# Kernel tuning notes

Measured on AMD Instinct MI355X. Metric: run time of the kernel, lower is better.

## Reference

```python
import jax, jax.numpy as jnp
import numpy as np

N, E, D, C = 100000, 3200000, 256, 47


def _l2norm(x):
    n = jnp.sqrt(jnp.sum(x * x, axis=-1, keepdims=True))
    return x / jnp.maximum(n, 1e-12)


def setup_inputs() -> dict:
    key = jax.random.key(0)
    ks = jax.random.split(key, 12)
    w = lambda k, s: jax.random.normal(k, s, dtype=jnp.float32) * 0.05
    return {
        "x": jax.random.normal(ks[0], (N, D), dtype=jnp.float32),
        "src": jax.random.randint(ks[1], (E,), 0, N, dtype=jnp.int32),
        "dst": jnp.sort(jax.random.randint(ks[2], (E,), 0, N, dtype=jnp.int32)),
        "W_pre": w(ks[3], (D, D)), "b_pre": jnp.zeros((D,), jnp.float32),
        "Wl1": w(ks[4], (D, D)), "bl1": jnp.zeros((D,), jnp.float32),
        "Wr1": w(ks[5], (D, D)),
        "Wl2": w(ks[6], (D, D)), "bl2": jnp.zeros((D,), jnp.float32),
        "Wr2": w(ks[7], (D, D)),
        "W_jk": w(ks[8], (D, D)), "b_jk": jnp.zeros((D,), jnp.float32),
        "W_post": w(ks[9], (C, D)), "b_post": jnp.zeros((C,), jnp.float32),
    }


def _sage_conv(x, src, dst, Wl, bl, Wr):
    # aggr='add': m_i = sum_{j in N(i)} x_j  (SpMM as gather + segment_sum)
    m = jax.ops.segment_sum(x[src], dst, num_segments=N)
    out = m @ Wl.T + bl + x @ Wr.T  # lin_l(aggr) + lin_r(root)
    return _l2norm(out)            # SAGEConv normalize=True


def reference(x, src, dst, W_pre, b_pre, Wl1, bl1, Wr1, Wl2, bl2, Wr2,
              W_jk, b_jk, W_post, b_post):
    # pre-MLP (1 layer) + classifier activation; dropout=0, batch_norm off
    h = jax.nn.relu(x @ W_pre.T + b_pre)
    h = _l2norm(h)  # self.normalize
    # GraphSAGE, jk='last': act+dropout after every conv, then jk lin
    h = jax.nn.relu(_sage_conv(h, src, dst, Wl1, bl1, Wr1))
    h = jax.nn.relu(_sage_conv(h, src, dst, Wl2, bl2, Wr2))
    h = h @ W_jk.T + b_jk
    # post: act + post-MLP (1 layer)
    h = jax.nn.relu(h)
    h = h @ W_post.T + b_post
    return jax.nn.log_softmax(h, axis=-1)
```

## Files before the change

### kernel.cpp

```cpp
#include <hip/hip_runtime.h>
#include <stdint.h>

#define DEV __device__ __forceinline__

typedef __attribute__((ext_vector_type(8))) short bh8;
typedef __attribute__((ext_vector_type(4))) float f4;
#define LDS_AS __attribute__((address_space(3)))
#define GLB_AS __attribute__((address_space(1)))

DEV unsigned short f2bf(float f) {
    union { float f; uint32_t u; } c; c.f = f;
    uint32_t u = c.u;
    uint32_t r = (u + 0x7fffu + ((u >> 16) & 1u)) >> 16;
    return (unsigned short)r;
}
DEV float bf2f(unsigned short h) {
    union { uint32_t u; float f; } c; c.u = ((uint32_t)h) << 16;
    return c.f;
}

DEV uint8_t f2fp8(float v) {
    const float vs = v * 256.f;
    union { float f; uint32_t u; } c; c.f = vs;
    const uint32_t u = c.u + 0x7ffffu + ((c.u >> 20) & 1u);
    const uint32_t f8 = (u >> 20) - 960u;
    return (vs < 0.015625f) ? (uint8_t)0 : (uint8_t)f8;
}
DEV float fp8w(uint32_t x) { union { uint32_t u; float f; } c; c.u = x; return c.f; }

DEV void gload16(const void* g, void* l) {
    __builtin_amdgcn_global_load_lds((const GLB_AS uint32_t*)g, (LDS_AS uint32_t*)l, 16, 0, 0);
}

__global__ __launch_bounds__(256) void prep_kernel(
    const float* __restrict__ w0, const float* __restrict__ w1, const float* __restrict__ w2,
    const float* __restrict__ w3, const float* __restrict__ w4, const float* __restrict__ w5,
    unsigned short* __restrict__ wbBase,
    const int* __restrict__ dst, int* __restrict__ rp, int N, int E) {
    const int b = blockIdx.x;
    if (b < 384) {
        const int wi = b >> 6;
        const int i = (b & 63) * 256 + threadIdx.x;
        const float* s = wi == 0 ? w0 : wi == 1 ? w1 : wi == 2 ? w2 : wi == 3 ? w3 : wi == 4 ? w4 : w5;
        const float4 v = ((const float4*)s)[i];
        ushort4 o; o.x = f2bf(v.x); o.y = f2bf(v.y); o.z = f2bf(v.z); o.w = f2bf(v.w);
        ((ushort4*)(wbBase + (size_t)wi * 65536))[i] = o;
    } else {
        const int i = (b - 384) * 256 + threadIdx.x;
        if (i <= N) {
            int lo = 0, hi = E;
            while (lo < hi) { int mid = (lo + hi) >> 1; if (dst[mid] < i) lo = mid + 1; else hi = mid; }
            rp[i] = lo;
        }
    }
}

__global__ __launch_bounds__(256) void agg_fp8_kernel(const uint32_t* __restrict__ h32,
                                                      const int* __restrict__ src,
                                                      const int* __restrict__ rp,
                                                      unsigned short* __restrict__ mout, int nNodes) {
    const int node = blockIdx.x * 4 + (threadIdx.x >> 6);
    if (node >= nNodes) return;
    const int lane = threadIdx.x & 63;
    const int beg = __builtin_amdgcn_readfirstlane(rp[node]);
    const int end = __builtin_amdgcn_readfirstlane(rp[node + 1]);
    float a0 = 0.f, a1 = 0.f, a2 = 0.f, a3 = 0.f;
    int e = beg;
    for (; e + 8 <= end; e += 8) {
        int s[8];
#pragma unroll
        for (int i = 0; i < 8; i++) s[i] = src[e + i];
        uint32_t w[8];
#pragma unroll
        for (int i = 0; i < 8; i++) w[i] = h32[(size_t)s[i] * 64 + lane];
#pragma unroll
        for (int i = 0; i < 8; i++) {
            a0 += fp8w((w[i] << 20) & 0x07f00000u);
            a1 += fp8w((w[i] << 12) & 0x07f00000u);
            a2 += fp8w((w[i] << 4)  & 0x07f00000u);
            a3 += fp8w((w[i] >> 4)  & 0x07f00000u);
        }
    }
    for (; e < end; ++e) {
        const uint32_t w = h32[(size_t)src[e] * 64 + lane];
        a0 += fp8w((w << 20) & 0x07f00000u);
        a1 += fp8w((w << 12) & 0x07f00000u);
        a2 += fp8w((w << 4)  & 0x07f00000u);
        a3 += fp8w((w >> 4)  & 0x07f00000u);
    }
    const float sc = 0x1p112f;
    ushort4 o;
    o.x = f2bf(a0 * sc); o.y = f2bf(a1 * sc); o.z = f2bf(a2 * sc); o.w = f2bf(a3 * sc);
    *(ushort4*)&mout[(size_t)node * 256 + (size_t)lane * 4] = o;
}

__global__ __launch_bounds__(256) void agg_kernel(const unsigned short* __restrict__ h,
                                                  const int* __restrict__ src,
                                                  const int* __restrict__ rp,
                                                  unsigned short* __restrict__ mout, int nNodes) {
    const int node = blockIdx.x * 4 + (threadIdx.x >> 6);
    if (node >= nNodes) return;
    const int lane = threadIdx.x & 63;
    const size_t fo = (size_t)lane * 4;
    const int beg = __builtin_amdgcn_readfirstlane(rp[node]);
    const int end = __builtin_amdgcn_readfirstlane(rp[node + 1]);
    float a0 = 0.f, a1 = 0.f, a2 = 0.f, a3 = 0.f;
    int e = beg;
    for (; e + 4 <= end; e += 4) {
        const int s0 = src[e], s1 = src[e+1], s2 = src[e+2], s3 = src[e+3];
        ushort4 v0 = *(const ushort4*)&h[(size_t)s0 * 256 + fo];
        ushort4 v1 = *(const ushort4*)&h[(size_t)s1 * 256 + fo];
        ushort4 v2 = *(const ushort4*)&h[(size_t)s2 * 256 + fo];
        ushort4 v3 = *(const ushort4*)&h[(size_t)s3 * 256 + fo];
        a0 += bf2f(v0.x) + bf2f(v1.x) + bf2f(v2.x) + bf2f(v3.x);
        a1 += bf2f(v0.y) + bf2f(v1.y) + bf2f(v2.y) + bf2f(v3.y);
        a2 += bf2f(v0.z) + bf2f(v1.z) + bf2f(v2.z) + bf2f(v3.z);
        a3 += bf2f(v0.w) + bf2f(v1.w) + bf2f(v2.w) + bf2f(v3.w);
    }
    for (; e < end; ++e) {
        const int s = src[e];
        ushort4 v = *(const ushort4*)&h[(size_t)s * 256 + fo];
        a0 += bf2f(v.x); a1 += bf2f(v.y); a2 += bf2f(v.z); a3 += bf2f(v.w);
    }
    ushort4 o;
    o.x = f2bf(a0); o.y = f2bf(a1); o.z = f2bf(a2); o.w = f2bf(a3);
    *(ushort4*)&mout[(size_t)node * 256 + fo] = o;
}

template <int NSEG, int EPMODE, bool EMIT, bool CVT>
__global__ __launch_bounds__(512) void gemm_kernel(
    const void* __restrict__ A0v, const unsigned short* __restrict__ A1,
    const unsigned short* __restrict__ B0, const unsigned short* __restrict__ B1,
    const float* __restrict__ bias, unsigned short* __restrict__ Out,
    uint8_t* __restrict__ F8, int M) {
    __shared__ unsigned short Alds[2 * 128 * 32];
    __shared__ unsigned short Blds[2 * 256 * 32];
    __shared__ float ssq_lds[8][64];

    const unsigned short* A0 = (const unsigned short*)A0v;
    const float* A0f = (const float*)A0v;

    const int t = threadIdx.x;
    const int wid = t >> 6;
    const int lane = t & 63;
    const int wr = wid >> 2, wc = wid & 3;
    const int l15 = lane & 15;
    const int kh = lane >> 4;
    const int rowBase = blockIdx.x * 128;

    f4 acc[4][4];
#pragma unroll
    for (int m = 0; m < 4; m++)
#pragma unroll
        for (int n = 0; n < 4; n++) acc[m][n] = f4{0.f, 0.f, 0.f, 0.f};

    const int rA = t >> 2;
    const int sSlotA = (t & 3) ^ ((rA >> 1) & 3);
    int grA = rowBase + rA; if (grA > M - 1) grA = M - 1;
    const size_t gAoff = (size_t)grA * 256 + sSlotA * 8;
    const size_t gBoff0 = (size_t)rA * 256 + sSlotA * 8;
    const size_t gBoff1 = (size_t)(128 + rA) * 256 + sSlotA * 8;

    const int nsteps = NSEG * 8;
    auto STAGE = [&](int s, int buf) {
        const unsigned short* Bp = (NSEG == 2 && s >= 8) ? B1 : B0;
        const int k0 = (s & 7) * 32;
        if (CVT) {
            const float* Af = A0f + gAoff + k0;
            const float4 v0 = *(const float4*)Af;
            const float4 v1 = *(const float4*)(Af + 4);
            bh8 o;
            o[0] = (short)f2bf(v0.x); o[1] = (short)f2bf(v0.y);
            o[2] = (short)f2bf(v0.z); o[3] = (short)f2bf(v0.w);
            o[4] = (short)f2bf(v1.x); o[5] = (short)f2bf(v1.y);
            o[6] = (short)f2bf(v1.z); o[7] = (short)f2bf(v1.w);
            *(bh8*)&Alds[buf * 4096 + wid * 512 + lane * 8] = o;
        } else {
            const unsigned short* Ap = (NSEG == 2 && s >= 8) ? A1 : A0;
            gload16(Ap + gAoff + k0, &Alds[buf * 4096 + wid * 512]);
        }
        gload16(Bp + gBoff0 + k0, &Blds[buf * 8192 + wid * 512]);
        gload16(Bp + gBoff1 + k0, &Blds[buf * 8192 + 4096 + wid * 512]);
    };

    STAGE(0, 0);
    asm volatile("s_waitcnt vmcnt(0)" ::: "memory");
    __syncthreads();

#pragma unroll 2
    for (int s = 0; s < nsteps; ++s) {
        const int cur = s & 1;
        if (s + 1 < nsteps) STAGE(s + 1, cur ^ 1);
        bh8 a[4], b[4];
#pragma unroll
        for (int m = 0; m < 4; m++) {
            const int ra = wr * 64 + m * 16 + l15;
            a[m] = *(const bh8*)&Alds[cur * 4096 + ra * 32 + ((kh ^ ((ra >> 1) & 3)) * 8)];
        }
#pragma unroll
        for (int n = 0; n < 4; n++) {
            const int rb = wc * 64 + n * 16 + l15;
            b[n] = *(const bh8*)&Blds[cur * 8192 + rb * 32 + ((kh ^ ((rb >> 1) & 3)) * 8)];
        }
#pragma unroll
        for (int m = 0; m < 4; m++)
#pragma unroll
            for (int n = 0; n < 4; n++)
                acc[m][n] = __builtin_amdgcn_mfma_f32_16x16x32_bf16(a[m], b[n], acc[m][n], 0, 0, 0);
        asm volatile("s_waitcnt vmcnt(0)" ::: "memory");
        __syncthreads();
    }

    const int cBase = wc * 64 + l15;
    float sq[4][4];
#pragma unroll
    for (int m = 0; m < 4; m++) { sq[m][0] = 0.f; sq[m][1] = 0.f; sq[m][2] = 0.f; sq[m][3] = 0.f; }
#pragma unroll
    for (int n = 0; n < 4; n++) {
        const float bv = bias[cBase + n * 16];
#pragma unroll
        for (int m = 0; m < 4; m++)
#pragma unroll
            for (int r = 0; r < 4; r++) {
                float v = acc[m][n][r] + bv;
                if (EPMODE != 1) v = fmaxf(v, 0.f);
                acc[m][n][r] = v;
                sq[m][r] += v * v;
            }
    }

    if (EPMODE != 2) {
#pragma unroll
        for (int mask = 1; mask < 16; mask <<= 1)
#pragma unroll
            for (int m = 0; m < 4; m++)
#pragma unroll
                for (int r = 0; r < 4; r++) sq[m][r] += __shfl_xor(sq[m][r], mask);
        if (l15 == 0) {
#pragma unroll
            for (int m = 0; m < 4; m++)
#pragma unroll
                for (int r = 0; r < 4; r++) ssq_lds[wid][m * 16 + kh * 4 + r] = sq[m][r];
        }
        __syncthreads();
#pragma unroll
        for (int m = 0; m < 4; m++)
#pragma unroll
            for (int r = 0; r < 4; r++) {
                const int rr = m * 16 + kh * 4 + r;
                const float s = ssq_lds[wr * 4 + 0][rr] + ssq_lds[wr * 4 + 1][rr] +
                                ssq_lds[wr * 4 + 2][rr] + ssq_lds[wr * 4 + 3][rr];
                sq[m][r] = 1.f / fmaxf(sqrtf(s), 1e-12f);
            }
    }

#pragma unroll
    for (int m = 0; m < 4; m++)
#pragma unroll
        for (int r = 0; r < 4; r++) {
            const int grow = rowBase + wr * 64 + m * 16 + kh * 4 + r;
            if (grow < M) {
#pragma unroll
                for (int n = 0; n < 4; n++) {
                    float v = acc[m][n][r];
                    if (EPMODE != 2) v *= sq[m][r];
                    if (EPMODE == 1) v = fmaxf(v, 0.f);
                    Out[(size_t)grow * 256 + cBase + n * 16] = f2bf(v);
                    if (EMIT) F8[(size_t)grow * 256 + cBase + n * 16] = f2fp8(v);
                }
            }
        }
}

__global__ __launch_bounds__(256) void jkfinal_kernel(
    const unsigned short* __restrict__ A,
    const unsigned short* __restrict__ Bjk,
    const float* __restrict__ bjk,
    const float* __restrict__ Wp, const float* __restrict__ bp,
    float* __restrict__ out, int M) {
    __shared__ unsigned short S[20480];
    __shared__ unsigned short Tlds[64 * 256];

    const int t = threadIdx.x;
    const int wid = t >> 6;
    const int lane = t & 63;
    const int wc = wid;
    const int l15 = lane & 15;
    const int kh = lane >> 4;
    const int rowBase = blockIdx.x * 64;

    f4 acc[4][4];
#pragma unroll
    for (int m = 0; m < 4; m++)
#pragma unroll
        for (int n = 0; n < 4; n++) acc[m][n] = f4{0.f, 0.f, 0.f, 0.f};

    const int rA = t >> 2;
    const int sSlotA = (t & 3) ^ ((rA >> 1) & 3);
    int grA = rowBase + rA; if (grA > M - 1) grA = M - 1;
    const size_t gAoff = (size_t)grA * 256 + sSlotA * 8;
    const size_t gBoff = (size_t)rA * 256 + sSlotA * 8;

    auto STAGE = [&](int s, int buf) {
        const int k0 = s * 32;
        gload16(A + gAoff + k0, &S[buf * 2048 + wid * 512]);
#pragma unroll
        for (int p = 0; p < 4; ++p)
            gload16(Bjk + (size_t)p * 16384 + gBoff + k0,
                    &S[4096 + buf * 8192 + p * 2048 + wid * 512]);
    };

    STAGE(0, 0);
    asm volatile("s_waitcnt vmcnt(0)" ::: "memory");
    __syncthreads();

#pragma unroll 2
    for (int s = 0; s < 8; ++s) {
        const int cur = s & 1;
        if (s + 1 < 8) STAGE(s + 1, cur ^ 1);
        bh8 a[4], b[4];
#pragma unroll
        for (int m = 0; m < 4; m++) {
            const int ra = m * 16 + l15;
            a[m] = *(const bh8*)&S[cur * 2048 + ra * 32 + ((kh ^ ((ra >> 1) & 3)) * 8)];
        }
#pragma unroll
        for (int n = 0; n < 4; n++) {
            const int rb = wc * 64 + n * 16 + l15;
            b[n] = *(const bh8*)&S[4096 + cur * 8192 + rb * 32 + ((kh ^ ((rb >> 1) & 3)) * 8)];
        }
#pragma unroll
        for (int m = 0; m < 4; m++)
#pragma unroll
            for (int n = 0; n < 4; n++)
                acc[m][n] = __builtin_amdgcn_mfma_f32_16x16x32_bf16(a[m], b[n], acc[m][n], 0, 0, 0);
        asm volatile("s_waitcnt vmcnt(0)" ::: "memory");
        __syncthreads();
    }

    const int cBase = wc * 64 + l15;
#pragma unroll
    for (int n = 0; n < 4; n++) {
        const float bv = bjk[cBase + n * 16];
        const int slot = wc * 4 + n;
#pragma unroll
        for (int m = 0; m < 4; m++)
#pragma unroll
            for (int r = 0; r < 4; r++) {
                const int row = m * 16 + kh * 4 + r;
                const float v = fmaxf(acc[m][n][r] + bv, 0.f);
                Tlds[row * 256 + (((slot ^ ((row >> 2) & 7)) << 4) | l15)] = f2bf(v);
            }
    }
    for (int i = t; i < 48 * 32; i += 256) {
        const int rb = i >> 5, slot = i & 31;
        bh8 o;
        if (rb < 47) {
#pragma unroll
            for (int j = 0; j < 8; j++) o[j] = (short)f2bf(Wp[rb * 256 + slot * 8 + j]);
        } else {
#pragma unroll
            for (int j = 0; j < 8; j++) o[j] = 0;
        }
        *(bh8*)&S[rb * 256 + ((slot ^ (rb & 7)) * 8)] = o;
    }
    __syncthreads();

    const int lrow = wid * 16 + l15;
    bh8 a2[8];
#pragma unroll
    for (int ks = 0; ks < 8; ks++) {
        const int slot = ks * 2 + (kh >> 1);
        a2[ks] = *(const bh8*)&Tlds[lrow * 256 + (((slot ^ ((lrow >> 2) & 7)) << 4) | ((kh & 1) * 8))];
    }
    f4 acc2[3];
#pragma unroll
    for (int n = 0; n < 3; n++) acc2[n] = f4{0.f, 0.f, 0.f, 0.f};
#pragma unroll
    for (int ks = 0; ks < 8; ks++)
#pragma unroll
        for (int n = 0; n < 3; n++) {
            const int rb = n * 16 + l15;
            const bh8 b = *(const bh8*)&S[rb * 256 + (((ks * 4 + kh) ^ (rb & 7)) * 8)];
            acc2[n] = __builtin_amdgcn_mfma_f32_16x16x32_bf16(a2[ks], b, acc2[n], 0, 0, 0);
        }

    const int c0 = l15, c1 = 16 + l15, c2 = 32 + l15;
    const float b0 = bp[c0], b1 = bp[c1];
    const float b2 = (l15 < 15) ? bp[c2] : 0.f;
#pragma unroll
    for (int r = 0; r < 4; r++) {
        const int grow = rowBase + wid * 16 + kh * 4 + r;
        const float x0 = acc2[0][r] + b0;
        const float x1 = acc2[1][r] + b1;
        const float x2 = (l15 < 15) ? (acc2[2][r] + b2) : -3.0e38f;
        float mx = fmaxf(fmaxf(x0, x1), x2);
#pragma unroll
        for (int msk = 1; msk < 16; msk <<= 1) mx = fmaxf(mx, __shfl_xor(mx, msk));
        float se = __expf(x0 - mx) + __expf(x1 - mx) + ((l15 < 15) ? __expf(x2 - mx) : 0.f);
#pragma unroll
        for (int msk = 1; msk < 16; msk <<= 1) se += __shfl_xor(se, msk);
        const float ls = __logf(se) + mx;
        if (grow < M) {
            float* orow = &out[(size_t)grow * 47];
            orow[c0] = x0 - ls;
            orow[c1] = x1 - ls;
            if (l15 < 15) orow[c2] = x2 - ls;
        }
    }
}

extern "C" void kernel_launch(void* const* d_in, const int* in_sizes, int n_in,
                              void* d_out, int out_size, void* d_ws, size_t ws_size,
                              hipStream_t stream) {
    const float* x      = (const float*)d_in[0];
    const int*   src    = (const int*)d_in[1];
    const int*   dst    = (const int*)d_in[2];
    const float* W_pre  = (const float*)d_in[3];
    const float* b_pre  = (const float*)d_in[4];
    const float* Wl1    = (const float*)d_in[5];
    const float* bl1    = (const float*)d_in[6];
    const float* Wr1    = (const float*)d_in[7];
    const float* Wl2    = (const float*)d_in[8];
    const float* bl2    = (const float*)d_in[9];
    const float* Wr2    = (const float*)d_in[10];
    const float* W_jk   = (const float*)d_in[11];
    const float* b_jk   = (const float*)d_in[12];
    const float* W_post = (const float*)d_in[13];
    const float* b_post = (const float*)d_in[14];

    const int N = in_sizes[0] / 256;
    const int E = in_sizes[1];

    char* ws = (char*)d_ws;
    char* ws0 = ws;
    const size_t HB = (size_t)N * 256 * 2;
    unsigned short* bufA = (unsigned short*)ws; ws += HB;
    unsigned short* bufB = (unsigned short*)ws; ws += HB;
    unsigned short* bufC = (unsigned short*)ws; ws += HB;
    unsigned short* bufD = (unsigned short*)ws; ws += HB;
    unsigned short* wbBase = (unsigned short*)ws; ws += (size_t)6 * 65536 * 2;
    int* rp = (int*)ws; ws += (size_t)(N + 1) * 4;
    uint8_t* f8 = (uint8_t*)ws; ws += (size_t)N * 256;
    const bool useFp8 = ((size_t)(ws - ws0) <= ws_size);

    const int nbr = (N + 1 + 255) / 256;
    prep_kernel<<<384 + nbr, 256, 0, stream>>>(W_pre, Wl1, Wr1, Wl2, Wr2, W_jk,
                                               wbBase, dst, rp, N, E);
    unsigned short* wb[6];
    for (int i = 0; i < 6; i++) wb[i] = wbBase + (size_t)i * 65536;

    const int gB = (N + 127) / 128;
    const int gAgg = (N + 3) / 4;
    if (useFp8) {
        gemm_kernel<1, 0, true, true><<<gB, 512, 0, stream>>>(x, nullptr, wb[0], nullptr, b_pre, bufB, f8, N);
        agg_fp8_kernel<<<gAgg, 256, 0, stream>>>((const uint32_t*)f8, src, rp, bufC, N);
        gemm_kernel<2, 1, true, false><<<gB, 512, 0, stream>>>(bufC, bufB, wb[1], wb[2], bl1, bufD, f8, N);
        agg_fp8_kernel<<<gAgg, 256, 0, stream>>>((const uint32_t*)f8, src, rp, bufC, N);
        gemm_kernel<2, 1, false, false><<<gB, 512, 0, stream>>>(bufC, bufD, wb[3], wb[4], bl2, bufA, nullptr, N);
    } else {
        gemm_kernel<1, 0, false, true><<<gB, 512, 0, stream>>>(x, nullptr, wb[0], nullptr, b_pre, bufB, nullptr, N);
        agg_kernel<<<gAgg, 256, 0, stream>>>(bufB, src, rp, bufC, N);
        gemm_kernel<2, 1, false, false><<<gB, 512, 0, stream>>>(bufC, bufB, wb[1], wb[2], bl1, bufD, nullptr, N);
        agg_kernel<<<gAgg, 256, 0, stream>>>(bufD, src, rp, bufC, N);
        gemm_kernel<2, 1, false, false><<<gB, 512, 0, stream>>>(bufC, bufD, wb[3], wb[4], bl2, bufA, nullptr, N);
    }
    jkfinal_kernel<<<(N + 63) / 64, 256, 0, stream>>>(bufA, wb[5], b_jk, W_post, b_post,
                                                      (float*)d_out, N);
}
```

Measured before the change: 587.3 us.

## Store intermediate activations only as FP8 and decode to bf16 on load

The GEMM kernels now write their normalized outputs only as FP8 bytes instead of both bf16 and FP8. Downstream consumers (the root-term segment of the next GEMM and the JK/final kernel) read the FP8 buffers and decode to bf16 in registers before staging into LDS. This halves the bytes written and read for the root activations, and uses two ping-pong FP8 buffers. In exchange it adds more quantization error on the root path, and those loads switch from async global_load_lds to register loads plus conversion.

```diff
diff --git a/kernel.cpp b/kernel.cpp
--- a/kernel.cpp
+++ b/kernel.cpp
@@ -27,6 +27,9 @@
     return (vs < 0.015625f) ? (uint8_t)0 : (uint8_t)f8;
 }
 DEV float fp8w(uint32_t x) { union { uint32_t u; float f; } c; c.u = x; return c.f; }
+DEV unsigned short fp82bf(uint32_t f) {
+    return f ? (unsigned short)((f << 4) + 0x3800u) : (unsigned short)0;
+}
 
 DEV void gload16(const void* g, void* l) {
     __builtin_amdgcn_global_load_lds((const GLB_AS uint32_t*)g, (LDS_AS uint32_t*)l, 16, 0, 0);
@@ -127,9 +130,9 @@
     *(ushort4*)&mout[(size_t)node * 256 + fo] = o;
 }
 
-template <int NSEG, int EPMODE, bool EMIT, bool CVT>
+template <int NSEG, int EPMODE, bool OUTF8, bool A0CVT, bool A1F8>
 __global__ __launch_bounds__(512) void gemm_kernel(
-    const void* __restrict__ A0v, const unsigned short* __restrict__ A1,
+    const void* __restrict__ A0v, const void* __restrict__ A1v,
     const unsigned short* __restrict__ B0, const unsigned short* __restrict__ B1,
     const float* __restrict__ bias, unsigned short* __restrict__ Out,
     uint8_t* __restrict__ F8, int M) {
@@ -137,13 +140,12 @@
     __shared__ unsigned short Blds[2 * 256 * 32];
     __shared__ float ssq_lds[8][64];
 
-    const unsigned short* A0 = (const unsigned short*)A0v;
-    const float* A0f = (const float*)A0v;
-
     const int t = threadIdx.x;
     const int wid = t >> 6;
     const int lane = t & 63;
-    const int wr = wid >> 2, wc = wid & 3;
+    const int wr = wid >> 1 >> 1 >> 0, wcDummy = 0; (void)wcDummy;
+    const int wr2 = wid >> 2, wc = wid & 3;
+    (void)wr;
     const int l15 = lane & 15;
     const int kh = lane >> 4;
     const int rowBase = blockIdx.x * 128;
@@ -165,19 +167,34 @@
     auto STAGE = [&](int s, int buf) {
         const unsigned short* Bp = (NSEG == 2 && s >= 8) ? B1 : B0;
         const int k0 = (s & 7) * 32;
-        if (CVT) {
-            const float* Af = A0f + gAoff + k0;
-            const float4 v0 = *(const float4*)Af;
-            const float4 v1 = *(const float4*)(Af + 4);
-            bh8 o;
-            o[0] = (short)f2bf(v0.x); o[1] = (short)f2bf(v0.y);
-            o[2] = (short)f2bf(v0.z); o[3] = (short)f2bf(v0.w);
-            o[4] = (short)f2bf(v1.x); o[5] = (short)f2bf(v1.y);
-            o[6] = (short)f2bf(v1.z); o[7] = (short)f2bf(v1.w);
-            *(bh8*)&Alds[buf * 4096 + wid * 512 + lane * 8] = o;
+        const bool seg1 = (NSEG == 2 && s >= 8);
+        if (!seg1) {
+            if (A0CVT) {
+                const float* Af = (const float*)A0v + gAoff + k0;
+                const float4 v0 = *(const float4*)Af;
+                const float4 v1 = *(const float4*)(Af + 4);
+                bh8 o;
+                o[0] = (short)f2bf(v0.x); o[1] = (short)f2bf(v0.y);
+                o[2] = (short)f2bf(v0.z); o[3] = (short)f2bf(v0.w);
+                o[4] = (short)f2bf(v1.x); o[5] = (short)f2bf(v1.y);
+                o[6] = (short)f2bf(v1.z); o[7] = (short)f2bf(v1.w);
+                *(bh8*)&Alds[buf * 4096 + wid * 512 + lane * 8] = o;
+            } else {
+                gload16((const unsigned short*)A0v + gAoff + k0, &Alds[buf * 4096 + wid * 512]);
+            }
         } else {
-            const unsigned short* Ap = (NSEG == 2 && s >= 8) ? A1 : A0;
-            gload16(Ap + gAoff + k0, &Alds[buf * 4096 + wid * 512]);
+            if (A1F8) {
+                const uint8_t* Ab = (const uint8_t*)A1v;
+                const uint2 p = *(const uint2*)&Ab[gAoff + k0];
+                bh8 o;
+                o[0] = (short)fp82bf(p.x & 0xffu);         o[1] = (short)fp82bf((p.x >> 8) & 0xffu);
+                o[2] = (short)fp82bf((p.x >> 16) & 0xffu); o[3] = (short)fp82bf((p.x >> 24) & 0xffu);
+                o[4] = (short)fp82bf(p.y & 0xffu);         o[5] = (short)fp82bf((p.y >> 8) & 0xffu);
+                o[6] = (short)fp82bf((p.y >> 16) & 0xffu); o[7] = (short)fp82bf((p.y >> 24) & 0xffu);
+                *(bh8*)&Alds[buf * 4096 + wid * 512 + lane * 8] = o;
+            } else {
+                gload16((const unsigned short*)A1v + gAoff + k0, &Alds[buf * 4096 + wid * 512]);
+            }
         }
         gload16(Bp + gBoff0 + k0, &Blds[buf * 8192 + wid * 512]);
         gload16(Bp + gBoff1 + k0, &Blds[buf * 8192 + 4096 + wid * 512]);
@@ -194,7 +211,7 @@
         bh8 a[4], b[4];
 #pragma unroll
         for (int m = 0; m < 4; m++) {
-            const int ra = wr * 64 + m * 16 + l15;
+            const int ra = wr2 * 64 + m * 16 + l15;
             a[m] = *(const bh8*)&Alds[cur * 4096 + ra * 32 + ((kh ^ ((ra >> 1) & 3)) * 8)];
         }
 #pragma unroll
@@ -248,8 +265,8 @@
 #pragma unroll
             for (int r = 0; r < 4; r++) {
                 const int rr = m * 16 + kh * 4 + r;
-                const float s = ssq_lds[wr * 4 + 0][rr] + ssq_lds[wr * 4 + 1][rr] +
-                                ssq_lds[wr * 4 + 2][rr] + ssq_lds[wr * 4 + 3][rr];
+                const float s = ssq_lds[wr2 * 4 + 0][rr] + ssq_lds[wr2 * 4 + 1][rr] +
+                                ssq_lds[wr2 * 4 + 2][rr] + ssq_lds[wr2 * 4 + 3][rr];
                 sq[m][r] = 1.f / fmaxf(sqrtf(s), 1e-12f);
             }
     }
@@ -258,22 +275,23 @@
     for (int m = 0; m < 4; m++)
 #pragma unroll
         for (int r = 0; r < 4; r++) {
-            const int grow = rowBase + wr * 64 + m * 16 + kh * 4 + r;
+            const int grow = rowBase + wr2 * 64 + m * 16 + kh * 4 + r;
             if (grow < M) {
 #pragma unroll
                 for (int n = 0; n < 4; n++) {
                     float v = acc[m][n][r];
                     if (EPMODE != 2) v *= sq[m][r];
                     if (EPMODE == 1) v = fmaxf(v, 0.f);
-                    Out[(size_t)grow * 256 + cBase + n * 16] = f2bf(v);
-                    if (EMIT) F8[(size_t)grow * 256 + cBase + n * 16] = f2fp8(v);
+                    if (OUTF8) F8[(size_t)grow * 256 + cBase + n * 16] = f2fp8(v);
+                    else       Out[(size_t)grow * 256 + cBase + n * 16] = f2bf(v);
                 }
             }
         }
 }
 
+template <bool AF8>
 __global__ __launch_bounds__(256) void jkfinal_kernel(
-    const unsigned short* __restrict__ A,
+    const void* __restrict__ Av,
     const unsigned short* __restrict__ Bjk,
     const float* __restrict__ bjk,
     const float* __restrict__ Wp, const float* __restrict__ bp,
@@ -303,7 +321,18 @@
 
     auto STAGE = [&](int s, int buf) {
         const int k0 = s * 32;
-        gload16(A + gAoff + k0, &S[buf * 2048 + wid * 512]);
+        if (AF8) {
+            const uint8_t* Ab = (const uint8_t*)Av;
+            const uint2 p = *(const uint2*)&Ab[gAoff + k0];
+            bh8 o;
+            o[0] = (short)fp82bf(p.x & 0xffu);         o[1] = (short)fp82bf((p.x >> 8) & 0xffu);
+            o[2] = (short)fp82bf((p.x >> 16) & 0xffu); o[3] = (short)fp82bf((p.x >> 24) & 0xffu);
+            o[4] = (short)fp82bf(p.y & 0xffu);         o[5] = (short)fp82bf((p.y >> 8) & 0xffu);
+            o[6] = (short)fp82bf((p.y >> 16) & 0xffu); o[7] = (short)fp82bf((p.y >> 24) & 0xffu);
+            *(bh8*)&S[buf * 2048 + wid * 512 + lane * 8] = o;
+        } else {
+            gload16((const unsigned short*)Av + gAoff + k0, &S[buf * 2048 + wid * 512]);
+        }
 #pragma unroll
         for (int p = 0; p < 4; ++p)
             gload16(Bjk + (size_t)p * 16384 + gBoff + k0,
@@ -441,7 +470,8 @@
     unsigned short* bufD = (unsigned short*)ws; ws += HB;
     unsigned short* wbBase = (unsigned short*)ws; ws += (size_t)6 * 65536 * 2;
     int* rp = (int*)ws; ws += (size_t)(N + 1) * 4;
-    uint8_t* f8 = (uint8_t*)ws; ws += (size_t)N * 256;
+    uint8_t* f8A = (uint8_t*)ws; ws += (size_t)N * 256;
+    uint8_t* f8B = (uint8_t*)ws; ws += (size_t)N * 256;
     const bool useFp8 = ((size_t)(ws - ws0) <= ws_size);
 
     const int nbr = (N + 1 + 255) / 256;
@@ -453,18 +483,20 @@
     const int gB = (N + 127) / 128;
     const int gAgg = (N + 3) / 4;
     if (useFp8) {
-        gemm_kernel<1, 0, true, true><<<gB, 512, 0, stream>>>(x, nullptr, wb[0], nullptr, b_pre, bufB, f8, N);
-        agg_fp8_kernel<<<gAgg, 256, 0, stream>>>((const uint32_t*)f8, src, rp, bufC, N);
-        gemm_kernel<2, 1, true, false><<<gB, 512, 0, stream>>>(bufC, bufB, wb[1], wb[2], bl1, bufD, f8, N);
-        agg_fp8_kernel<<<gAgg, 256, 0, stream>>>((const uint32_t*)f8, src, rp, bufC, N);
-        gemm_kernel<2, 1, false, false><<<gB, 512, 0, stream>>>(bufC, bufD, wb[3], wb[4], bl2, bufA, nullptr, N);
+        gemm_kernel<1, 0, true, true, false><<<gB, 512, 0, stream>>>(x, nullptr, wb[0], nullptr, b_pre, nullptr, f8A, N);
+        agg_fp8_kernel<<<gAgg, 256, 0, stream>>>((const uint32_t*)f8A, src, rp, bufC, N);
+        gemm_kernel<2, 1, true, false, true><<<gB, 512, 0, stream>>>(bufC, f8A, wb[1], wb[2], bl1, nullptr, f8B, N);
+        agg_fp8_kernel<<<gAgg, 256, 0, stream>>>((const uint32_t*)f8B, src, rp, bufC, N);
+        gemm_kernel<2, 1, true, false, true><<<gB, 512, 0, stream>>>(bufC, f8B, wb[3], wb[4], bl2, nullptr, f8A, N);
+        jkfinal_kernel<true><<<(N + 63) / 64, 256, 0, stream>>>(f8A, wb[5], b_jk, W_post, b_post,
+                                                                (float*)d_out, N);
     } else {
-        gemm_kernel<1, 0, false, true><<<gB, 512, 0, stream>>>(x, nullptr, wb[0], nullptr, b_pre, bufB, nullptr, N);
+        gemm_kernel<1, 0, false, true, false><<<gB, 512, 0, stream>>>(x, nullptr, wb[0], nullptr, b_pre, bufB, nullptr, N);
         agg_kernel<<<gAgg, 256, 0, stream>>>(bufB, src, rp, bufC, N);
-        gemm_kernel<2, 1, false, false><<<gB, 512, 0, stream>>>(bufC, bufB, wb[1], wb[2], bl1, bufD, nullptr, N);
+        gemm_kernel<2, 1, false, false, false><<<gB, 512, 0, stream>>>(bufC, bufB, wb[1], wb[2], bl1, bufD, nullptr, N);
         agg_kernel<<<gAgg, 256, 0, stream>>>(bufD, src, rp, bufC, N);
-        gemm_kernel<2, 1, false, false><<<gB, 512, 0, stream>>>(bufC, bufD, wb[3], wb[4], bl2, bufA, nullptr, N);
-    }
-    jkfinal_kernel<<<(N + 63) / 64, 256, 0, stream>>>(bufA, wb[5], b_jk, W_post, b_post,
-                                                      (float*)d_out, N);
-}
+        gemm_kernel<2, 1, false, false, false><<<gB, 512, 0, stream>>>(bufC, bufD, wb[3], wb[4], bl2, bufA, nullptr, N);
+        jkfinal_kernel<false><<<(N + 63) / 64, 256, 0, stream>>>(bufA, wb[5], b_jk, W_post, b_post,
+                                                                 (float*)d_out, N);
+    }
+}
```

Measured after the change: 573.8 us. 2.3% less time.
